# Optimization experiments

Hardware: AMD Instinct MI355X
Metric: run time of the kernel (lower is better)

The kernel has to match this reference:

```python
import jax, jax.numpy as jnp
import numpy as np

DIM = 2048
N_HEADS = 32
N_KV_HEADS = 8
HEAD_DIM = 64
REPEATS = N_HEADS // N_KV_HEADS
SCALE = HEAD_DIM ** -0.5
L = 2048
B = 1


def rotary_matrix(context_len, d):
    # Dense (L, d, d) RoPE rotation matrix, exactly as get_rotary_matrix1.
    pos = jnp.arange(1, context_len + 1, dtype=jnp.float32)[:, None]
    i = jnp.arange(d // 2)
    theta = 10000.0 ** (-2.0 * i.astype(jnp.float32) / d)
    m_theta = pos * theta  # (L, d/2)
    cos_v, sin_v = jnp.cos(m_theta), jnp.sin(m_theta)
    R = jnp.zeros((context_len, d, d), dtype=jnp.float32)
    R = R.at[:, 2 * i, 2 * i].set(cos_v)
    R = R.at[:, 2 * i, 2 * i + 1].set(-sin_v)
    R = R.at[:, 2 * i + 1, 2 * i].set(sin_v)
    R = R.at[:, 2 * i + 1, 2 * i + 1].set(cos_v)
    return R


def causal_mask(context_len):
    idx = jnp.arange(context_len)
    return (idx[:, None] < idx[None, :]).astype(jnp.float32) * -1e9


def setup_inputs() -> dict:
    key = jax.random.key(0)
    ks = jax.random.split(key, 5)
    x = jax.random.normal(ks[0], (B, L, DIM), dtype=jnp.float32)
    mask = causal_mask(L)
    wq_w = jax.random.normal(ks[1], (N_HEADS * HEAD_DIM, DIM), dtype=jnp.float32) * 0.02
    wk_w = jax.random.normal(ks[2], (N_KV_HEADS * HEAD_DIM, DIM), dtype=jnp.float32) * 0.02
    wv_w = jax.random.normal(ks[3], (N_KV_HEADS * HEAD_DIM, DIM), dtype=jnp.float32) * 0.02
    wo_w = jax.random.normal(ks[4], (DIM, N_HEADS * HEAD_DIM), dtype=jnp.float32) * 0.02
    return {"x": x, "mask": mask, "wq_w": wq_w, "wk_w": wk_w, "wv_w": wv_w, "wo_w": wo_w}


def reference(x, mask, wq_w, wk_w, wv_w, wo_w):
    Bx, Lx, D = x.shape
    # projections (torch Linear: y = x @ W.T)
    q = jnp.einsum('bld,od->blo', x, wq_w).reshape(Bx, Lx, N_HEADS, HEAD_DIM).transpose(0, 2, 1, 3)
    k = jnp.einsum('bld,od->blo', x, wk_w).reshape(Bx, Lx, N_KV_HEADS, HEAD_DIM).transpose(0, 2, 1, 3)
    v = jnp.einsum('bld,od->blo', x, wv_w).reshape(Bx, Lx, N_KV_HEADS, HEAD_DIM).transpose(0, 2, 1, 3)
    # GQA repeat of kv heads (interleaved, matching concat-unsqueeze-reshape)
    k = jnp.repeat(k, REPEATS, axis=1)
    v = jnp.repeat(v, REPEATS, axis=1)
    # dense-matrix RoPE on q and (repeated) k
    R = rotary_matrix(Lx, HEAD_DIM)
    q = jnp.einsum('bhlj,lij->bhli', q, R)
    k = jnp.einsum('bhlj,lij->bhli', k, R)
    scores = jnp.einsum('bhld,bhmd->bhlm', q, k) * SCALE + mask
    attn = jax.nn.softmax(scores.astype(jnp.float32), axis=-1)
    out = jnp.einsum('bhlm,bhmd->bhld', attn, v)
    out = out.transpose(0, 2, 1, 3).reshape(Bx, Lx, N_HEADS * HEAD_DIM)
    out = jnp.einsum('blo,do->bld', out, wo_w)
    return out, k, v
```

## Files before the change

kernel.cpp:

```cpp
#include <hip/hip_runtime.h>

typedef __bf16 bf16;
typedef __bf16 bf16x8 __attribute__((ext_vector_type(8)));
typedef float floatx4 __attribute__((ext_vector_type(4)));
typedef float floatx16 __attribute__((ext_vector_type(16)));
typedef unsigned int uint;

#define MFMA16(a, b, c) __builtin_amdgcn_mfma_f32_16x16x32_bf16((a), (b), (c), 0, 0, 0)
#define MFMA32(a, b, c) __builtin_amdgcn_mfma_f32_32x32x16_bf16((a), (b), (c), 0, 0, 0)

__device__ __forceinline__ void gl2lds16(const bf16* g, bf16* l) {
  __builtin_amdgcn_global_load_lds(
      (const __attribute__((address_space(1))) void*)g,
      (__attribute__((address_space(3))) void*)l, 16, 0, 0);
}
__device__ __forceinline__ void wait_vm0() { __builtin_amdgcn_s_waitcnt(0x0f70); }

__device__ __forceinline__ void cvt8(const float* __restrict__ s,
                                     bf16* __restrict__ d, int i8) {
  const float4 a = ((const float4*)s)[i8 * 2];
  const float4 b = ((const float4*)s)[i8 * 2 + 1];
  bf16x8 o;
  o[0] = (bf16)a.x; o[1] = (bf16)a.y; o[2] = (bf16)a.z; o[3] = (bf16)a.w;
  o[4] = (bf16)b.x; o[5] = (bf16)b.y; o[6] = (bf16)b.z; o[7] = (bf16)b.w;
  *(bf16x8*)(d + i8 * 8) = o;
}

__global__ __launch_bounds__(256) void convert_kernel(
    const float* __restrict__ x, const float* __restrict__ wq,
    const float* __restrict__ wk, const float* __restrict__ wv,
    const float* __restrict__ wo, bf16* __restrict__ xb,
    bf16* __restrict__ wqb, bf16* __restrict__ wkb, bf16* __restrict__ wvb,
    bf16* __restrict__ wob) {
  const int g = blockIdx.x * 256 + threadIdx.x;
  if (g < 524288) cvt8(x, xb, g);
  else if (g < 1048576) cvt8(wq, wqb, g - 524288);
  else if (g < 1179648) cvt8(wk, wkb, g - 1048576);
  else if (g < 1310720) cvt8(wv, wvb, g - 1179648);
  else cvt8(wo, wob, g - 1310720);
}

template <typename OutT>
__device__ __forceinline__ void gemm_tile_body64(
    const bf16* __restrict__ A, int lda,
    const bf16* __restrict__ B, int ldb,
    OutT* __restrict__ C, int ldc, int K,
    bf16* S) {
  const int t = threadIdx.x;
  const int w = t >> 6, lane = t & 63;
  const int l15 = lane & 15, qd = lane >> 4;
  const int wr = w >> 1, wc = w & 1;

  floatx4 acc[2][4];
#pragma unroll
  for (int i = 0; i < 2; ++i)
#pragma unroll
    for (int j = 0; j < 4; ++j) acc[i][j] = (floatx4){0.f, 0.f, 0.f, 0.f};

  const bf16* gb[6];
  int lo[6];
#pragma unroll
  for (int i = 0; i < 6; ++i) {
    const int u = w + 4 * i;
    lo[i] = u * 512 + lane * 8;
    if (u < 8) {
      gb[i] = A + ((u >> 1) * 16 + l15) * lda + (u & 1) * 32 + qd * 8;
    } else {
      const int v = u - 8;
      gb[i] = B + ((v >> 1) * 16 + l15) * ldb + (v & 1) * 32 + qd * 8;
    }
  }

#define STG64(kt_, buf_)                                            \
  {                                                                 \
    bf16* d_ = S + (buf_) * 12288;                                  \
    _Pragma("unroll")                                               \
    for (int i_ = 0; i_ < 6; ++i_)                                  \
      gl2lds16(gb[i_] + (kt_) * 64, d_ + lo[i_]);                   \
  }

  const int NT = K >> 6;
  STG64(0, 0);
  wait_vm0();
  __syncthreads();
  int cur = 0;
  for (int kt = 0; kt < NT; ++kt) {
    if (kt + 1 < NT) STG64(kt + 1, cur ^ 1);
    const bf16* Ab = S + cur * 12288;
    const bf16* Bb = Ab + 4096;
    bf16x8 a[2][2], b[4][2];
#pragma unroll
    for (int i = 0; i < 2; ++i)
#pragma unroll
      for (int kk = 0; kk < 2; ++kk)
        a[i][kk] =
            *(const bf16x8*)(Ab + ((wr * 2 + i) * 2 + kk) * 512 + lane * 8);
#pragma unroll
    for (int j = 0; j < 4; ++j)
#pragma unroll
      for (int kk = 0; kk < 2; ++kk)
        b[j][kk] =
            *(const bf16x8*)(Bb + ((wc * 4 + j) * 2 + kk) * 512 + lane * 8);
#pragma unroll
    for (int kk = 0; kk < 2; ++kk)
#pragma unroll
      for (int i = 0; i < 2; ++i)
#pragma unroll
        for (int j = 0; j < 4; ++j)
          acc[i][j] = MFMA16(a[i][kk], b[j][kk], acc[i][j]);
    wait_vm0();
    __builtin_amdgcn_sched_barrier(0);
    __builtin_amdgcn_s_barrier();
    __builtin_amdgcn_sched_barrier(0);
    cur ^= 1;
  }
#undef STG64

#pragma unroll
  for (int i = 0; i < 2; ++i)
#pragma unroll
    for (int j = 0; j < 4; ++j) {
      const int row = wr * 32 + i * 16 + qd * 4;
      const int col = wc * 64 + j * 16 + l15;
#pragma unroll
      for (int r = 0; r < 4; ++r)
        C[(row + r) * ldc + col] = (OutT)acc[i][j][r];
    }
}

__global__ __launch_bounds__(256) void gemm_qkv(
    const bf16* __restrict__ x, const bf16* __restrict__ wq,
    const bf16* __restrict__ wk, const bf16* __restrict__ wv,
    bf16* __restrict__ Qws, bf16* __restrict__ Kh, bf16* __restrict__ Vh,
    bf16* __restrict__ Vt) {
  __shared__ bf16 SM[17152];
  bf16* As = SM;
  bf16* Bs = SM + 4096;
  const int bid = blockIdx.y * 24 + blockIdx.x;
  const int swz = (bid & 7) * 48 + (bid >> 3);
  const int nb = swz % 24;
  const int m0 = (swz / 24) * 128;
  const bf16* B;
  if (nb < 16) B = wq + nb * 128 * 2048;
  else if (nb < 20) B = wk + (nb - 16) * 128 * 2048;
  else B = wv + (nb - 20) * 128 * 2048;

  const int t = threadIdx.x;
  const int w = t >> 6, lane = t & 63;
  const int l15 = lane & 15, qd = lane >> 4;
  const int wr = w >> 1, wc = w & 1;

  floatx4 acc[4][4];
#pragma unroll
  for (int i = 0; i < 4; ++i)
#pragma unroll
    for (int j = 0; j < 4; ++j) acc[i][j] = (floatx4){0.f, 0.f, 0.f, 0.f};

  const bf16* A = x + m0 * 2048;
  const int mt0 = w, mt1 = w + 4;
  const int kseg = qd * 8;
  const bf16* ga0 = A + (mt0 * 16 + l15) * 2048 + kseg;
  const bf16* ga1 = A + (mt1 * 16 + l15) * 2048 + kseg;
  const bf16* gb0 = B + (mt0 * 16 + l15) * 2048 + kseg;
  const bf16* gb1 = B + (mt1 * 16 + l15) * 2048 + kseg;
  bf16* lA0 = As + mt0 * 512 + lane * 8;
  bf16* lA1 = As + mt1 * 512 + lane * 8;
  bf16* lB0 = Bs + mt0 * 512 + lane * 8;
  bf16* lB1 = Bs + mt1 * 512 + lane * 8;

  for (int k0 = 0; k0 < 2048; k0 += 32) {
    gl2lds16(ga0 + k0, lA0);
    gl2lds16(ga1 + k0, lA1);
    gl2lds16(gb0 + k0, lB0);
    gl2lds16(gb1 + k0, lB1);
    wait_vm0();
    __syncthreads();

    bf16x8 a[4], b[4];
#pragma unroll
    for (int i = 0; i < 4; ++i)
      a[i] = *(const bf16x8*)(As + (wr * 4 + i) * 512 + lane * 8);
#pragma unroll
    for (int j = 0; j < 4; ++j)
      b[j] = *(const bf16x8*)(Bs + (wc * 4 + j) * 512 + lane * 8);
#pragma unroll
    for (int i = 0; i < 4; ++i)
#pragma unroll
      for (int j = 0; j < 4; ++j) acc[i][j] = MFMA16(a[i], b[j], acc[i][j]);
    __syncthreads();
  }

#pragma unroll
  for (int i = 0; i < 4; ++i)
#pragma unroll
    for (int j = 0; j < 4; ++j) {
      const int row = wr * 64 + i * 16 + qd * 4;
      const int col = wc * 64 + j * 16 + l15;
#pragma unroll
      for (int r = 0; r < 4; ++r)
        SM[(row + r) * 134 + col] = (bf16)acc[i][j][r];
    }
  __syncthreads();

  const float NEG_LOG2_10000_D32 = -0.4152410118609203f;
  if (nb < 16) {
#pragma unroll
    for (int k = 0; k < 8; ++k) {
      const int u = t + (k << 8);
      const int row = u >> 4, c8 = (u & 15) << 3;
      const bf16x8 v = *(const bf16x8*)&SM[row * 134 + c8];
      const float base = (float)(m0 + row + 1);
      bf16x8 ov;
#pragma unroll
      for (int p = 0; p < 4; ++p) {
        const int a = ((c8 & 63) >> 1) + p;
        float s, c;
        __sincosf(base * exp2f(NEG_LOG2_10000_D32 * (float)a), &s, &c);
        const float x0 = (float)v[2 * p], x1 = (float)v[2 * p + 1];
        ov[2 * p] = (bf16)(c * x0 - s * x1);
        ov[2 * p + 1] = (bf16)(s * x0 + c * x1);
      }
      *(bf16x8*)&Qws[(m0 + row) * 2048 + nb * 128 + c8] = ov;
    }
  } else if (nb < 20) {
#pragma unroll
    for (int k = 0; k < 8; ++k) {
      const int u = t + (k << 8);
      const int row = u >> 4, c8 = (u & 15) << 3;
      const bf16x8 v = *(const bf16x8*)&SM[row * 134 + c8];
      const float base = (float)(m0 + row + 1);
      bf16x8 ov;
#pragma unroll
      for (int p = 0; p < 4; ++p) {
        const int a = ((c8 & 63) >> 1) + p;
        float s, c;
        __sincosf(base * exp2f(NEG_LOG2_10000_D32 * (float)a), &s, &c);
        const float x0 = (float)v[2 * p], x1 = (float)v[2 * p + 1];
        ov[2 * p] = (bf16)(c * x0 - s * x1);
        ov[2 * p + 1] = (bf16)(s * x0 + c * x1);
      }
      const int g512 = (nb - 16) * 128 + c8;
      const int kvh = g512 >> 6, d8 = g512 & 63;
      *(bf16x8*)&Kh[(kvh * 2048 + m0 + row) * 64 + d8] = ov;
    }
  } else {
#pragma unroll
    for (int k = 0; k < 8; ++k) {
      const int u = t + (k << 8);
      const int row = u >> 4, c8 = (u & 15) << 3;
      const bf16x8 v = *(const bf16x8*)&SM[row * 134 + c8];
      const int g512 = (nb - 20) * 128 + c8;
      const int kvh = g512 >> 6, d8 = g512 & 63;
      *(bf16x8*)&Vh[(kvh * 2048 + m0 + row) * 64 + d8] = v;
    }
#pragma unroll
    for (int k = 0; k < 8; ++k) {
      const int u = t + (k << 8);
      const int col = u >> 4, r8 = (u & 15) << 3;
      bf16x8 v;
#pragma unroll
      for (int jj = 0; jj < 8; ++jj) v[jj] = SM[(r8 + jj) * 134 + col];
      const int g512 = (nb - 20) * 128 + col;
      const int kvh = g512 >> 6, d = g512 & 63;
      *(bf16x8*)&Vt[kvh * 131072 + d * 2048 + m0 + r8] = v;
    }
  }
}

__global__ __launch_bounds__(256) void gemm_o(
    const bf16* __restrict__ Ows, const bf16* __restrict__ wo,
    float* __restrict__ out) {
  __shared__ bf16 S[24576];
  const int bid = blockIdx.y * 16 + blockIdx.x;
  const int swz = (bid & 7) * 64 + (bid >> 3);
  const int n0 = (swz & 15) * 128;
  const int m0 = (swz >> 4) * 64;
  gemm_tile_body64<float>(Ows + m0 * 2048, 2048, wo + n0 * 2048, 2048,
                          out + m0 * 2048 + n0, 2048, 2048, S);
}

__global__ __launch_bounds__(256) void flash_kernel(
    const bf16* __restrict__ Qws, const bf16* __restrict__ Kh,
    const bf16* __restrict__ Vh, const bf16* __restrict__ Vt,
    bf16* __restrict__ Ows, float* __restrict__ Opart, float* __restrict__ ML,
    float* __restrict__ kout, float* __restrict__ vout) {
  __shared__ bf16 KVs[2][2][4096];
  __shared__ bf16 Osh[128 * 66];

  const int h = blockIdx.y;
  const int bx = blockIdx.x;
  int qt, seg, kts, kte;
  if (bx < 8) {
    qt = bx; seg = -1; kts = 0; kte = 2 * qt + 2;
  } else {
    const int i = bx - 8;
    qt = 8 + (i >> 1);
    seg = i & 1;
    const int half = qt + 1;
    kts = seg * half;
    kte = kts + half;
  }
  const int kh = h >> 2;
  const int q0 = qt * 128;
  const int t = threadIdx.x, w = t >> 6, lane = t & 63;
  const int l31 = lane & 31, hf = lane >> 5;
  const int qw = q0 + w * 32;

  const int s0 = w, s1 = w + 4;
  const bf16* gK0 = Kh + kh * 131072 + ((s0 >> 2) * 32 + l31) * 64 + (s0 & 3) * 16 + hf * 8;
  const bf16* gK1 = Kh + kh * 131072 + ((s1 >> 2) * 32 + l31) * 64 + (s1 & 3) * 16 + hf * 8;
  const bf16* gV0 = Vt + kh * 131072 + ((s0 >> 2) * 32 + l31) * 2048 + (s0 & 3) * 16 + hf * 8;
  const bf16* gV1 = Vt + kh * 131072 + ((s1 >> 2) * 32 + l31) * 2048 + (s1 & 3) * 16 + hf * 8;

  {
    const int nb = kts & 1;
    gl2lds16(gK0 + kts * 4096, &KVs[nb][0][s0 * 512 + lane * 8]);
    gl2lds16(gK1 + kts * 4096, &KVs[nb][0][s1 * 512 + lane * 8]);
    gl2lds16(gV0 + kts * 64, &KVs[nb][1][s0 * 512 + lane * 8]);
    gl2lds16(gV1 + kts * 64, &KVs[nb][1][s1 * 512 + lane * 8]);
  }

  bf16x8 qf[4];
  {
    const bf16* qrow = Qws + (qw + l31) * 2048 + h * 64 + hf * 8;
#pragma unroll
    for (int c = 0; c < 4; ++c) qf[c] = *(const bf16x8*)(qrow + c * 16);
  }

  {
    const int bid = (int)blockIdx.y * 24 + (int)blockIdx.x;
    for (uint u = (uint)(bid * 256 + t); u < 262144u; u += 196608u) {
      const uint u2 = u & 131071u;
      const bf16* src = (u < 131072u) ? Kh : Vh;
      float* dst = (u < 131072u) ? kout : vout;
      const int kvh2 = u2 >> 14;
      const int rr = u2 & 16383;
      const int l = rr >> 3, d8 = (rr & 7) * 8;
      const bf16x8 v = *(const bf16x8*)(src + (kvh2 * 2048 + l) * 64 + d8);
      float4 f0, f1;
      f0.x = (float)v[0]; f0.y = (float)v[1]; f0.z = (float)v[2]; f0.w = (float)v[3];
      f1.x = (float)v[4]; f1.y = (float)v[5]; f1.z = (float)v[6]; f1.w = (float)v[7];
#pragma unroll
      for (int rep = 0; rep < 4; ++rep) {
        float* o2 = dst + (((kvh2 * 4 + rep) * 2048 + l) * 64 + d8);
        *(float4*)o2 = f0;
        *(float4*)(o2 + 4) = f1;
      }
    }
  }

  floatx16 o[2] = {};
  float mrun = -3e38f, lrun = 0.f;

  const float C = 0.1803368801f;
  for (int kt = kts; kt < kte; ++kt) {
    wait_vm0();
    __syncthreads();
    if (kt + 1 < kte) {
      const int nb = (kt + 1) & 1;
      const int koff = (kt + 1) * 4096, voff = (kt + 1) * 64;
      gl2lds16(gK0 + koff, &KVs[nb][0][s0 * 512 + lane * 8]);
      gl2lds16(gK1 + koff, &KVs[nb][0][s1 * 512 + lane * 8]);
      gl2lds16(gV0 + voff, &KVs[nb][1][s0 * 512 + lane * 8]);
      gl2lds16(gV1 + voff, &KVs[nb][1][s1 * 512 + lane * 8]);
    }
    const int kt64 = kt * 64;
    if (kt64 > qw + 31) continue;
    const bf16* Kb = &KVs[kt & 1][0][0];
    const bf16* Vb = &KVs[kt & 1][1][0];

    floatx16 st[2];
    __builtin_amdgcn_s_setprio(1);
#pragma unroll
    for (int tt = 0; tt < 2; ++tt) {
      floatx16 z = {};
#pragma unroll
      for (int c = 0; c < 4; ++c) {
        const bf16x8 kf = *(const bf16x8*)(Kb + (tt * 4 + c) * 512 + lane * 8);
        z = MFMA32(kf, qf[c], z);
      }
      st[tt] = z;
    }
    __builtin_amdgcn_s_setprio(0);
    if (kt64 + 64 > qw) {
      const int myq = qw + l31;
#pragma unroll
      for (int tt = 0; tt < 2; ++tt)
#pragma unroll
        for (int r = 0; r < 16; ++r) {
          const int key = kt64 + tt * 32 + (r & 3) + 8 * (r >> 2) + 4 * hf;
          if (key > myq) st[tt][r] = -1e30f;
        }
    }
    float ma = -3e38f, mb = -3e38f, mc = -3e38f, md = -3e38f;
#pragma unroll
    for (int tt = 0; tt < 2; ++tt)
#pragma unroll
      for (int r = 0; r < 16; r += 4) {
        ma = fmaxf(ma, st[tt][r + 0]);
        mb = fmaxf(mb, st[tt][r + 1]);
        mc = fmaxf(mc, st[tt][r + 2]);
        md = fmaxf(md, st[tt][r + 3]);
      }
    float mx = fmaxf(fmaxf(ma, mb), fmaxf(mc, md));
    mx = fmaxf(mx, __shfl_xor(mx, 32));
    const bool defer = __all((mx - mrun) * C <= 8.f);
    if (!defer) {
      const float mn = fmaxf(mrun, mx);
      const float al = __builtin_amdgcn_exp2f((mrun - mn) * C);
      lrun *= al;
#pragma unroll
      for (int n = 0; n < 2; ++n)
#pragma unroll
        for (int r = 0; r < 16; ++r) o[n][r] *= al;
      mrun = mn;
    }
    float ra = 0.f, rb = 0.f, rc = 0.f, rd = 0.f;
#pragma unroll
    for (int tt = 0; tt < 2; ++tt)
#pragma unroll
      for (int r = 0; r < 16; r += 4) {
        const float p0 = __builtin_amdgcn_exp2f((st[tt][r + 0] - mrun) * C);
        const float p1 = __builtin_amdgcn_exp2f((st[tt][r + 1] - mrun) * C);
        const float p2 = __builtin_amdgcn_exp2f((st[tt][r + 2] - mrun) * C);
        const float p3 = __builtin_amdgcn_exp2f((st[tt][r + 3] - mrun) * C);
        st[tt][r + 0] = p0; ra += p0;
        st[tt][r + 1] = p1; rb += p1;
        st[tt][r + 2] = p2; rc += p2;
        st[tt][r + 3] = p3; rd += p3;
      }
    float rs = (ra + rb) + (rc + rd);
    rs += __shfl_xor(rs, 32);
    lrun += rs;

    uint pk[2][4][2];
#pragma unroll
    for (int tt = 0; tt < 2; ++tt)
#pragma unroll
      for (int g = 0; g < 4; ++g)
#pragma unroll
        for (int p = 0; p < 2; ++p) {
          union { bf16 h2[2]; uint u; } cv;
          cv.h2[0] = (bf16)st[tt][4 * g + 2 * p];
          cv.h2[1] = (bf16)st[tt][4 * g + 2 * p + 1];
          pk[tt][g][p] = cv.u;
        }
    uint own_[2][2][2], rv[2][2][2];
#pragma unroll
    for (int tt = 0; tt < 2; ++tt)
#pragma unroll
      for (int gam = 0; gam < 2; ++gam)
#pragma unroll
        for (int p = 0; p < 2; ++p) {
          own_[tt][gam][p] = hf ? pk[tt][2 * gam + 1][p] : pk[tt][2 * gam][p];
          const uint snd = hf ? pk[tt][2 * gam][p] : pk[tt][2 * gam + 1][p];
          rv[tt][gam][p] = (uint)__shfl_xor((int)snd, 32);
        }
    __builtin_amdgcn_s_setprio(1);
#pragma unroll
    for (int c = 0; c < 4; ++c) {
      const int tt = c >> 1, gam = c & 1;
      union { uint u[4]; bf16x8 v; } pf;
      pf.u[0] = hf ? rv[tt][gam][0] : own_[tt][gam][0];
      pf.u[1] = hf ? rv[tt][gam][1] : own_[tt][gam][1];
      pf.u[2] = hf ? own_[tt][gam][0] : rv[tt][gam][0];
      pf.u[3] = hf ? own_[tt][gam][1] : rv[tt][gam][1];
#pragma unroll
      for (int n = 0; n < 2; ++n)
        o[n] = MFMA32(*(const bf16x8*)(Vb + (n * 4 + c) * 512 + lane * 8),
                      pf.v, o[n]);
    }
    __builtin_amdgcn_s_setprio(0);
  }

  if (seg < 0) {
    const float inv = 1.f / lrun;
#pragma unroll
    for (int n = 0; n < 2; ++n)
#pragma unroll
      for (int r = 0; r < 16; ++r) {
        const int dl = n * 32 + (r & 3) + 8 * (r >> 2) + 4 * hf;
        Osh[(w * 32 + l31) * 66 + dl] = (bf16)(o[n][r] * inv);
      }
    __syncthreads();
#pragma unroll
    for (int i = 0; i < 4; ++i) {
      const int row = (t >> 3) + i * 32;
      const int col = (t & 7) * 8;
      const bf16x8 vv = *(const bf16x8*)&Osh[row * 66 + col];
      *(bf16x8*)&Ows[(q0 + row) * 2048 + h * 64 + col] = vv;
    }
  } else {
    const int idx = (h * 8 + (qt - 8)) * 2 + seg;
    float* Op = Opart + idx * 8192;
#pragma unroll
    for (int n = 0; n < 2; ++n)
#pragma unroll
      for (int r = 0; r < 16; ++r) {
        const int dl = n * 32 + (r & 3) + 8 * (r >> 2) + 4 * hf;
        Op[dl * 128 + w * 32 + l31] = o[n][r];
      }
    if (hf == 0) {
      ML[idx * 256 + w * 32 + l31] = mrun;
      ML[idx * 256 + 128 + w * 32 + l31] = lrun;
    }
  }
}

__global__ __launch_bounds__(256) void combine_kernel(
    const float* __restrict__ Opart, const float* __restrict__ ML,
    bf16* __restrict__ Ows) {
  __shared__ bf16 Osh[128 * 66];
  const int b = blockIdx.x;
  const int h = b >> 3, qt = (b & 7) + 8;
  const int q0 = qt * 128;
  const int t = threadIdx.x;
  const int row = t & 127, dh = t >> 7;
  const int i0 = (h * 8 + (qt - 8)) * 2;
  const float C = 0.1803368801f;
  const float m0 = ML[i0 * 256 + row], l0 = ML[i0 * 256 + 128 + row];
  const float m1 = ML[(i0 + 1) * 256 + row], l1 = ML[(i0 + 1) * 256 + 128 + row];
  const float m = fmaxf(m0, m1);
  const float w0 = __builtin_amdgcn_exp2f((m0 - m) * C);
  const float w1 = __builtin_amdgcn_exp2f((m1 - m) * C);
  const float inv = 1.f / (l0 * w0 + l1 * w1);
  const float* P0 = Opart + i0 * 8192;
  const float* P1 = Opart + (i0 + 1) * 8192;
#pragma unroll
  for (int j = 0; j < 32; ++j) {
    const int d = dh * 32 + j;
    const float v = (P0[d * 128 + row] * w0 + P1[d * 128 + row] * w1) * inv;
    Osh[row * 66 + d] = (bf16)v;
  }
  __syncthreads();
#pragma unroll
  for (int i = 0; i < 4; ++i) {
    const int r2 = (t >> 3) + i * 32;
    const int col = (t & 7) * 8;
    const bf16x8 vv = *(const bf16x8*)&Osh[r2 * 66 + col];
    *(bf16x8*)&Ows[(q0 + r2) * 2048 + h * 64 + col] = vv;
  }
}

extern "C" void kernel_launch(void* const* d_in, const int* in_sizes, int n_in,
                              void* d_out, int out_size, void* d_ws,
                              size_t ws_size, hipStream_t stream) {
  const float* x = (const float*)d_in[0];
  const float* wq = (const float*)d_in[2];
  const float* wk = (const float*)d_in[3];
  const float* wv = (const float*)d_in[4];
  const float* wo = (const float*)d_in[5];

  float* out = (float*)d_out;
  float* kout = out + 4194304;
  float* vout = out + 8388608;

  bf16* ws = (bf16*)d_ws;
  bf16* xb = ws;
  bf16* wqb = xb + 4194304;
  bf16* wkb = wqb + 4194304;
  bf16* wvb = wkb + 1048576;
  bf16* wob = wvb + 1048576;
  bf16* Qws = wob + 4194304;
  bf16* Kws = Qws + 4194304;
  bf16* Vh = Kws + 1048576;
  bf16* Vt = Vh + 1048576;
  bf16* Ows = Vt + 1048576;
  bf16* Kh = Ows + 4194304;
  float* Opart = out;
  float* MLf = (float*)Kws;

  convert_kernel<<<dim3(7168), dim3(256), 0, stream>>>(x, wq, wk, wv, wo, xb,
                                                       wqb, wkb, wvb, wob);
  gemm_qkv<<<dim3(24, 16), dim3(256), 0, stream>>>(xb, wqb, wkb, wvb, Qws, Kh,
                                                   Vh, Vt);
  flash_kernel<<<dim3(24, 32), dim3(256), 0, stream>>>(Qws, Kh, Vh, Vt, Ows,
                                                       Opart, MLf, kout, vout);
  combine_kernel<<<dim3(256), dim3(256), 0, stream>>>(Opart, MLf, Ows);
  gemm_o<<<dim3(16, 32), dim3(256), 0, stream>>>(Ows, wob, out);
}
```

Measured before the change: 283.4 us.

## Rebalance flash split-KV work into 2/3 segments and move k/v export to gemm_o

Changes the flash-attention grid so mid query tiles split their KV range in two and late tiles in three, which spreads causal work more evenly across more blocks. The partial outputs now spill into both the output buffer and the workspace. The K/V fp32 expansion writes move from the flash prologue into the tail of the output GEMM, so flash blocks start compute sooner. LDS is merged into one shared array, reusing the KV buffer for the output staging. In exchange, the combine kernel must merge up to three partials per tile, which adds more partial-result traffic, and gemm_o gains a store-heavy epilogue.

```diff
diff --git a/kernel.cpp b/kernel.cpp
--- a/kernel.cpp
+++ b/kernel.cpp
@@ -15,6 +15,14 @@
       (__attribute__((address_space(3))) void*)l, 16, 0, 0);
 }
 __device__ __forceinline__ void wait_vm0() { __builtin_amdgcn_s_waitcnt(0x0f70); }
+
+__device__ __forceinline__ float* slot_ptr(int s, float* o0, float* o1) {
+  return s < 512 ? o0 + (size_t)s * 8192 : o1 + (size_t)(s - 512) * 8192;
+}
+__device__ __forceinline__ const float* slot_ptr_c(int s, const float* o0,
+                                                   const float* o1) {
+  return s < 512 ? o0 + (size_t)s * 8192 : o1 + (size_t)(s - 512) * 8192;
+}
 
 __device__ __forceinline__ void cvt8(const float* __restrict__ s,
                                      bf16* __restrict__ d, int i8) {
@@ -269,7 +277,9 @@
 
 __global__ __launch_bounds__(256) void gemm_o(
     const bf16* __restrict__ Ows, const bf16* __restrict__ wo,
-    float* __restrict__ out) {
+    float* __restrict__ out, const bf16* __restrict__ Kh,
+    const bf16* __restrict__ Vh, float* __restrict__ kout,
+    float* __restrict__ vout) {
   __shared__ bf16 S[24576];
   const int bid = blockIdx.y * 16 + blockIdx.x;
   const int swz = (bid & 7) * 64 + (bid >> 3);
@@ -277,28 +287,51 @@
   const int m0 = (swz >> 4) * 64;
   gemm_tile_body64<float>(Ows + m0 * 2048, 2048, wo + n0 * 2048, 2048,
                           out + m0 * 2048 + n0, 2048, 2048, S);
+
+  const int g = bid * 256 + (int)threadIdx.x;
+  for (uint u = (uint)g; u < 262144u; u += 131072u) {
+    const uint u2 = u & 131071u;
+    const bf16* src = (u < 131072u) ? Kh : Vh;
+    float* dst = (u < 131072u) ? kout : vout;
+    const int kvh2 = u2 >> 14;
+    const int rr = u2 & 16383;
+    const int l = rr >> 3, d8 = (rr & 7) * 8;
+    const bf16x8 v = *(const bf16x8*)(src + (kvh2 * 2048 + l) * 64 + d8);
+    float4 f0, f1;
+    f0.x = (float)v[0]; f0.y = (float)v[1]; f0.z = (float)v[2]; f0.w = (float)v[3];
+    f1.x = (float)v[4]; f1.y = (float)v[5]; f1.z = (float)v[6]; f1.w = (float)v[7];
+#pragma unroll
+    for (int rep = 0; rep < 4; ++rep) {
+      float* o2 = dst + (((kvh2 * 4 + rep) * 2048 + l) * 64 + d8);
+      *(float4*)o2 = f0;
+      *(float4*)(o2 + 4) = f1;
+    }
+  }
 }
 
 __global__ __launch_bounds__(256) void flash_kernel(
     const bf16* __restrict__ Qws, const bf16* __restrict__ Kh,
-    const bf16* __restrict__ Vh, const bf16* __restrict__ Vt,
-    bf16* __restrict__ Ows, float* __restrict__ Opart, float* __restrict__ ML,
-    float* __restrict__ kout, float* __restrict__ vout) {
-  __shared__ bf16 KVs[2][2][4096];
-  __shared__ bf16 Osh[128 * 66];
+    const bf16* __restrict__ Vt, bf16* __restrict__ Ows,
+    float* __restrict__ Op0, float* __restrict__ Op1, float* __restrict__ ML) {
+  __shared__ bf16 SMEM[16384];
 
   const int h = blockIdx.y;
   const int bx = blockIdx.x;
-  int qt, seg, kts, kte;
-  if (bx < 8) {
-    qt = bx; seg = -1; kts = 0; kte = 2 * qt + 2;
+  int qt, seg, kts, kte, slot;
+  if (bx < 4) {
+    qt = bx; seg = -1; kts = 0; kte = 2 * qt + 2; slot = -1;
+  } else if (bx < 12) {
+    const int j = bx - 4;
+    qt = 4 + (j >> 1); seg = j & 1;
+    const int nkt = 2 * qt + 2;
+    kts = seg * nkt / 2; kte = (seg + 1) * nkt / 2;
+    slot = h * 32 + (bx - 4);
   } else {
-    const int i = bx - 8;
-    qt = 8 + (i >> 1);
-    seg = i & 1;
-    const int half = qt + 1;
-    kts = seg * half;
-    kte = kts + half;
+    const int j = bx - 12;
+    qt = 8 + j / 3; seg = j % 3;
+    const int nkt = 2 * qt + 2;
+    kts = seg * nkt / 3; kte = (seg + 1) * nkt / 3;
+    slot = h * 32 + (bx - 4);
   }
   const int kh = h >> 2;
   const int q0 = qt * 128;
@@ -314,10 +347,10 @@
 
   {
     const int nb = kts & 1;
-    gl2lds16(gK0 + kts * 4096, &KVs[nb][0][s0 * 512 + lane * 8]);
-    gl2lds16(gK1 + kts * 4096, &KVs[nb][0][s1 * 512 + lane * 8]);
-    gl2lds16(gV0 + kts * 64, &KVs[nb][1][s0 * 512 + lane * 8]);
-    gl2lds16(gV1 + kts * 64, &KVs[nb][1][s1 * 512 + lane * 8]);
+    gl2lds16(gK0 + kts * 4096, &SMEM[nb * 8192 + s0 * 512 + lane * 8]);
+    gl2lds16(gK1 + kts * 4096, &SMEM[nb * 8192 + s1 * 512 + lane * 8]);
+    gl2lds16(gV0 + kts * 64, &SMEM[nb * 8192 + 4096 + s0 * 512 + lane * 8]);
+    gl2lds16(gV1 + kts * 64, &SMEM[nb * 8192 + 4096 + s1 * 512 + lane * 8]);
   }
 
   bf16x8 qf[4];
@@ -325,28 +358,6 @@
     const bf16* qrow = Qws + (qw + l31) * 2048 + h * 64 + hf * 8;
 #pragma unroll
     for (int c = 0; c < 4; ++c) qf[c] = *(const bf16x8*)(qrow + c * 16);
-  }
-
-  {
-    const int bid = (int)blockIdx.y * 24 + (int)blockIdx.x;
-    for (uint u = (uint)(bid * 256 + t); u < 262144u; u += 196608u) {
-      const uint u2 = u & 131071u;
-      const bf16* src = (u < 131072u) ? Kh : Vh;
-      float* dst = (u < 131072u) ? kout : vout;
-      const int kvh2 = u2 >> 14;
-      const int rr = u2 & 16383;
-      const int l = rr >> 3, d8 = (rr & 7) * 8;
-      const bf16x8 v = *(const bf16x8*)(src + (kvh2 * 2048 + l) * 64 + d8);
-      float4 f0, f1;
-      f0.x = (float)v[0]; f0.y = (float)v[1]; f0.z = (float)v[2]; f0.w = (float)v[3];
-      f1.x = (float)v[4]; f1.y = (float)v[5]; f1.z = (float)v[6]; f1.w = (float)v[7];
-#pragma unroll
-      for (int rep = 0; rep < 4; ++rep) {
-        float* o2 = dst + (((kvh2 * 4 + rep) * 2048 + l) * 64 + d8);
-        *(float4*)o2 = f0;
-        *(float4*)(o2 + 4) = f1;
-      }
-    }
   }
 
   floatx16 o[2] = {};
@@ -359,15 +370,15 @@
     if (kt + 1 < kte) {
       const int nb = (kt + 1) & 1;
       const int koff = (kt + 1) * 4096, voff = (kt + 1) * 64;
-      gl2lds16(gK0 + koff, &KVs[nb][0][s0 * 512 + lane * 8]);
-      gl2lds16(gK1 + koff, &KVs[nb][0][s1 * 512 + lane * 8]);
-      gl2lds16(gV0 + voff, &KVs[nb][1][s0 * 512 + lane * 8]);
-      gl2lds16(gV1 + voff, &KVs[nb][1][s1 * 512 + lane * 8]);
+      gl2lds16(gK0 + koff, &SMEM[nb * 8192 + s0 * 512 + lane * 8]);
+      gl2lds16(gK1 + koff, &SMEM[nb * 8192 + s1 * 512 + lane * 8]);
+      gl2lds16(gV0 + voff, &SMEM[nb * 8192 + 4096 + s0 * 512 + lane * 8]);
+      gl2lds16(gV1 + voff, &SMEM[nb * 8192 + 4096 + s1 * 512 + lane * 8]);
     }
     const int kt64 = kt * 64;
     if (kt64 > qw + 31) continue;
-    const bf16* Kb = &KVs[kt & 1][0][0];
-    const bf16* Vb = &KVs[kt & 1][1][0];
+    const bf16* Kb = &SMEM[(kt & 1) * 8192];
+    const bf16* Vb = Kb + 4096;
 
     floatx16 st[2];
     __builtin_amdgcn_s_setprio(1);
@@ -474,6 +485,8 @@
   }
 
   if (seg < 0) {
+    __syncthreads();
+    bf16* Osh = SMEM;
     const float inv = 1.f / lrun;
 #pragma unroll
     for (int n = 0; n < 2; ++n)
@@ -491,8 +504,7 @@
       *(bf16x8*)&Ows[(q0 + row) * 2048 + h * 64 + col] = vv;
     }
   } else {
-    const int idx = (h * 8 + (qt - 8)) * 2 + seg;
-    float* Op = Opart + idx * 8192;
+    float* Op = slot_ptr(slot, Op0, Op1);
 #pragma unroll
     for (int n = 0; n < 2; ++n)
 #pragma unroll
@@ -501,35 +513,43 @@
         Op[dl * 128 + w * 32 + l31] = o[n][r];
       }
     if (hf == 0) {
-      ML[idx * 256 + w * 32 + l31] = mrun;
-      ML[idx * 256 + 128 + w * 32 + l31] = lrun;
+      ML[slot * 256 + w * 32 + l31] = mrun;
+      ML[slot * 256 + 128 + w * 32 + l31] = lrun;
     }
   }
 }
 
 __global__ __launch_bounds__(256) void combine_kernel(
-    const float* __restrict__ Opart, const float* __restrict__ ML,
-    bf16* __restrict__ Ows) {
+    const float* __restrict__ Op0, const float* __restrict__ Op1,
+    const float* __restrict__ ML, bf16* __restrict__ Ows) {
   __shared__ bf16 Osh[128 * 66];
   const int b = blockIdx.x;
-  const int h = b >> 3, qt = (b & 7) + 8;
+  const int h = b / 12, qi = b % 12;
+  const int qt = 4 + qi;
   const int q0 = qt * 128;
+  const bool three = (qi >= 4);
+  const int slot0 = h * 32 + (three ? 8 + (qi - 4) * 3 : qi * 2);
   const int t = threadIdx.x;
   const int row = t & 127, dh = t >> 7;
-  const int i0 = (h * 8 + (qt - 8)) * 2;
   const float C = 0.1803368801f;
-  const float m0 = ML[i0 * 256 + row], l0 = ML[i0 * 256 + 128 + row];
-  const float m1 = ML[(i0 + 1) * 256 + row], l1 = ML[(i0 + 1) * 256 + 128 + row];
-  const float m = fmaxf(m0, m1);
+  const float m0 = ML[(slot0 + 0) * 256 + row], l0 = ML[(slot0 + 0) * 256 + 128 + row];
+  const float m1 = ML[(slot0 + 1) * 256 + row], l1 = ML[(slot0 + 1) * 256 + 128 + row];
+  const float m2 = three ? ML[(slot0 + 2) * 256 + row] : -3e38f;
+  const float l2 = three ? ML[(slot0 + 2) * 256 + 128 + row] : 0.f;
+  const float m = fmaxf(fmaxf(m0, m1), m2);
   const float w0 = __builtin_amdgcn_exp2f((m0 - m) * C);
   const float w1 = __builtin_amdgcn_exp2f((m1 - m) * C);
-  const float inv = 1.f / (l0 * w0 + l1 * w1);
-  const float* P0 = Opart + i0 * 8192;
-  const float* P1 = Opart + (i0 + 1) * 8192;
+  const float w2 = three ? __builtin_amdgcn_exp2f((m2 - m) * C) : 0.f;
+  const float inv = 1.f / (l0 * w0 + l1 * w1 + l2 * w2);
+  const float* P0 = slot_ptr_c(slot0 + 0, Op0, Op1);
+  const float* P1 = slot_ptr_c(slot0 + 1, Op0, Op1);
+  const float* P2 = three ? slot_ptr_c(slot0 + 2, Op0, Op1) : P0;
 #pragma unroll
   for (int j = 0; j < 32; ++j) {
     const int d = dh * 32 + j;
-    const float v = (P0[d * 128 + row] * w0 + P1[d * 128 + row] * w1) * inv;
+    const float v = (P0[d * 128 + row] * w0 + P1[d * 128 + row] * w1 +
+                     P2[d * 128 + row] * w2) *
+                    inv;
     Osh[row * 66 + d] = (bf16)v;
   }
   __syncthreads();
@@ -567,15 +587,17 @@
   bf16* Vt = Vh + 1048576;
   bf16* Ows = Vt + 1048576;
   bf16* Kh = Ows + 4194304;
-  float* Opart = out;
+  float* Op0 = out;
+  float* Op1 = (float*)ws;
   float* MLf = (float*)Kws;
 
   convert_kernel<<<dim3(7168), dim3(256), 0, stream>>>(x, wq, wk, wv, wo, xb,
                                                        wqb, wkb, wvb, wob);
   gemm_qkv<<<dim3(24, 16), dim3(256), 0, stream>>>(xb, wqb, wkb, wvb, Qws, Kh,
                                                    Vh, Vt);
-  flash_kernel<<<dim3(24, 32), dim3(256), 0, stream>>>(Qws, Kh, Vh, Vt, Ows,
-                                                       Opart, MLf, kout, vout);
-  combine_kernel<<<dim3(256), dim3(256), 0, stream>>>(Opart, MLf, Ows);
-  gemm_o<<<dim3(16, 32), dim3(256), 0, stream>>>(Ows, wob, out);
-}
+  flash_kernel<<<dim3(36, 32), dim3(256), 0, stream>>>(Qws, Kh, Vt, Ows, Op0,
+                                                       Op1, MLf);
+  combine_kernel<<<dim3(384), dim3(256), 0, stream>>>(Op0, Op1, MLf, Ows);
+  gemm_o<<<dim3(16, 32), dim3(256), 0, stream>>>(Ows, wob, out, Kh, Vh, kout,
+                                                 vout);
+}
```

Result: no change. 282.1 us (-0.5%).
